# Optimization experiments

Hardware: AMD Instinct MI355X
Metric: run time of the kernel (lower is better)

## Reference

```python
import jax, jax.numpy as jnp
import numpy as np
from functools import partial

L, E, H, FF = 6, 768, 12, 3072
D = E // H
EPS = 1e-5

def _layernorm(x, g, b):
    mu = jnp.mean(x, axis=-1, keepdims=True)
    var = jnp.mean(jnp.square(x - mu), axis=-1, keepdims=True)
    return (x - mu) * jax.lax.rsqrt(var + EPS) * g + b

def setup_inputs() -> dict:
    key = jax.random.key(0)
    ks = jax.random.split(key, 16)
    s = 0.02
    return {
        "inputs_embeds": jax.random.normal(ks[0], (2, 1024, E), jnp.float32),
        "attention_mask": jnp.ones((2, 1024), jnp.float32),
        "Wqkv": jax.random.normal(ks[1], (L, E, 3 * E), jnp.float32) * s,
        "bqkv": jnp.zeros((L, 3 * E), jnp.float32),
        "Wo": jax.random.normal(ks[2], (L, E, E), jnp.float32) * s,
        "bo": jnp.zeros((L, E), jnp.float32),
        "ln1_g": jnp.ones((L, E), jnp.float32),
        "ln1_b": jnp.zeros((L, E), jnp.float32),
        "ln2_g": jnp.ones((L, E), jnp.float32),
        "ln2_b": jnp.zeros((L, E), jnp.float32),
        "Wfc": jax.random.normal(ks[3], (L, E, FF), jnp.float32) * s,
        "bfc": jnp.zeros((L, FF), jnp.float32),
        "Wmo": jax.random.normal(ks[4], (L, FF, E), jnp.float32) * s,
        "bmo": jnp.zeros((L, E), jnp.float32),
        "lnf_g": jnp.ones((E,), jnp.float32),
        "lnf_b": jnp.zeros((E,), jnp.float32),
    }

def reference(inputs_embeds, attention_mask, Wqkv, bqkv, Wo, bo,
              ln1_g, ln1_b, ln2_g, ln2_b, Wfc, bfc, Wmo, bmo, lnf_g, lnf_b):
    B, S, _ = inputs_embeds.shape
    # additive mask, broadcast over heads and query positions: [B,1,1,S]
    mask_add = (1.0 - attention_mask)[:, None, None, :] * -10000.0
    scale = 1.0 / jnp.sqrt(jnp.float32(D))

    def block(x, p):
        wqkv, bq, wo_, bo_, g1, b1, g2, b2, wfc, bf, wmo, bm = p
        h = _layernorm(x, g1, b1)
        qkv = h @ wqkv + bq                      # [B,S,3E]
        q, k, v = jnp.split(qkv, 3, axis=-1)
        q = q.reshape(B, S, H, D).transpose(0, 2, 1, 3)  # [B,H,S,D]
        k = k.reshape(B, S, H, D).transpose(0, 2, 1, 3)
        v = v.reshape(B, S, H, D).transpose(0, 2, 1, 3)
        scores = jnp.einsum('bhqd,bhkd->bhqk', q, k) * scale + mask_add
        w = jax.nn.softmax(scores, axis=-1)
        a = jnp.einsum('bhqk,bhkd->bhqd', w, v)
        a = a.transpose(0, 2, 1, 3).reshape(B, S, E)
        x = x + a @ wo_ + bo_
        m = _layernorm(x, g2, b2)
        m = jax.nn.gelu(m @ wfc + bf, approximate=False) @ wmo + bm
        x = x + m
        return x, None

    params = (Wqkv, bqkv, Wo, bo, ln1_g, ln1_b, ln2_g, ln2_b, Wfc, bfc, Wmo, bmo)
    x, _ = jax.lax.scan(block, inputs_embeds, params)
    return _layernorm(x, lnf_g, lnf_b)
```

## Files before the change

kernel.cpp:

```cpp
#include <hip/hip_runtime.h>
#include <hip/hip_bf16.h>
#include <math.h>

constexpr int LYR = 6;
constexpr int E   = 768;
constexpr int NH  = 12;
constexpr int FFD = 3072;
constexpr int HD  = 64;
constexpr int BB  = 2;
constexpr int SS  = 1024;
constexpr int T   = BB * SS;
constexpr int E3  = 3 * E;
constexpr int FH  = FFD / 2;

constexpr size_t SZ_QKV_T = (size_t)E3 * E;
constexpr size_t SZ_WO_T  = (size_t)E * E;
constexpr size_t SZ_WFC_T = (size_t)FFD * E;
constexpr size_t SZ_WMO_T = (size_t)E * FFD;
constexpr size_t LSZ      = SZ_QKV_T + SZ_WO_T + SZ_WFC_T + SZ_WMO_T;
constexpr int TQ = (E3 / 64) * (E / 64);
constexpr int TO = (E / 64) * (E / 64);
constexpr int TF = (FFD / 64) * (E / 64);
constexpr int TM = (E / 64) * (FFD / 64);
constexpr int TL = TQ + TO + TF + TM;

#define LN_EPS 1e-5f

typedef __attribute__((ext_vector_type(8))) short    short8v;
typedef __attribute__((ext_vector_type(8))) unsigned short ushort8v;
typedef __attribute__((ext_vector_type(4))) unsigned short ushort4v;
typedef __attribute__((ext_vector_type(4))) float    f32x4;

__device__ __forceinline__ float bf2f(__hip_bfloat16 x) { return __bfloat162float(x); }
__device__ __forceinline__ float bfr2f(unsigned short u) {
    union { unsigned int i; float f; } v; v.i = ((unsigned int)u) << 16; return v.f;
}
__device__ __forceinline__ __hip_bfloat16 f2bf(float f) { return __float2bfloat16(f); }
__device__ __forceinline__ unsigned short f2bfbits(float f) {
    union { float f; unsigned int i; } v; v.f = f;
    unsigned int r = (v.i + 0x7fffu + ((v.i >> 16) & 1u)) >> 16;
    return (unsigned short)r;
}

__device__ __forceinline__ float block_sum(float v, float* sm) {
    #pragma unroll
    for (int o = 32; o > 0; o >>= 1) v += __shfl_down(v, o, 64);
    int lane = threadIdx.x & 63, wid = threadIdx.x >> 6;
    if (lane == 0) sm[wid] = v;
    __syncthreads();
    float r = sm[0] + sm[1] + sm[2] + sm[3];
    __syncthreads();
    return r;
}

__device__ __forceinline__ float block_max(float v, float* sm) {
    #pragma unroll
    for (int o = 32; o > 0; o >>= 1) v = fmaxf(v, __shfl_down(v, o, 64));
    int lane = threadIdx.x & 63, wid = threadIdx.x >> 6;
    if (lane == 0) sm[wid] = v;
    __syncthreads();
    float r = fmaxf(fmaxf(sm[0], sm[1]), fmaxf(sm[2], sm[3]));
    __syncthreads();
    return r;
}

__global__ void copy4_kernel(const float4* __restrict__ in, float4* __restrict__ out, int n4) {
    int i = blockIdx.x * 256 + threadIdx.x;
    if (i < n4) out[i] = in[i];
}

__global__ void rowstat_kernel(const float* __restrict__ x, float2* __restrict__ musig) {
    __shared__ float sm[4];
    int row = blockIdx.x;
    const float* xr = x + (size_t)row * E;
    float s = 0.f;
    for (int i = threadIdx.x; i < E; i += 256) s += xr[i];
    float mu = block_sum(s, sm) * (1.0f / E);
    float v = 0.f;
    for (int i = threadIdx.x; i < E; i += 256) { float d = xr[i] - mu; v += d * d; }
    float rstd = rsqrtf(block_sum(v, sm) * (1.0f / E) + LN_EPS);
    if (threadIdx.x == 0) musig[row] = make_float2(mu, rstd);
}

template <typename OT>
__global__ void ln_kernel(const float* __restrict__ x, OT* __restrict__ out,
                          const float* __restrict__ g, const float* __restrict__ b) {
    __shared__ float sm[4];
    int row = blockIdx.x;
    const float* xr = x + (size_t)row * E;
    float s = 0.f;
    for (int i = threadIdx.x; i < E; i += 256) s += xr[i];
    float mu = block_sum(s, sm) * (1.0f / E);
    float v = 0.f;
    for (int i = threadIdx.x; i < E; i += 256) { float d = xr[i] - mu; v += d * d; }
    float rstd = rsqrtf(block_sum(v, sm) * (1.0f / E) + LN_EPS);
    for (int i = threadIdx.x; i < E; i += 256) {
        float o = (xr[i] - mu) * rstd * g[i] + b[i];
        if constexpr (sizeof(OT) == 2) out[(size_t)row * E + i] = f2bf(o);
        else                           out[(size_t)row * E + i] = o;
    }
}

__device__ __forceinline__ void transpose_tile(const float* __restrict__ W,
                                               unsigned short* __restrict__ Wt,
                                               int K, int N, int n0, int k0) {
    __shared__ float tile[32][33];
    int tx = threadIdx.x & 31, ty = threadIdx.x >> 5;
    #pragma unroll
    for (int i = 0; i < 4; i++)
        tile[ty + i * 8][tx] = W[(size_t)(k0 + ty + i * 8) * N + n0 + tx];
    __syncthreads();
    #pragma unroll
    for (int i = 0; i < 4; i++)
        Wt[(size_t)(n0 + ty + i * 8) * K + k0 + tx] = f2bfbits(tile[tx][ty + i * 8]);
}

__global__ void transpose_cvt(const float* __restrict__ W, unsigned short* __restrict__ Wt,
                              int K, int N) {
    transpose_tile(W, Wt, K, N, blockIdx.x * 32, blockIdx.y * 32);
}

__device__ __forceinline__ void transpose_tile64(const float* __restrict__ W,
                                                 unsigned short* __restrict__ Wt,
                                                 int K, int N, int n0, int k0) {
    __shared__ float tile[64][65];
    int tid = threadIdx.x;
    int rr = tid >> 4, c4 = (tid & 15) * 4;
    #pragma unroll
    for (int i = 0; i < 4; i++) {
        float4 v = *(const float4*)&W[(size_t)(k0 + rr + i * 16) * N + n0 + c4];
        tile[rr + i * 16][c4 + 0] = v.x;
        tile[rr + i * 16][c4 + 1] = v.y;
        tile[rr + i * 16][c4 + 2] = v.z;
        tile[rr + i * 16][c4 + 3] = v.w;
    }
    __syncthreads();
    int nr = tid >> 3, kc = (tid & 7) * 8;
    #pragma unroll
    for (int i = 0; i < 2; i++) {
        int n = nr + i * 32;
        ushort8v o;
        #pragma unroll
        for (int e = 0; e < 8; e++) o[e] = f2bfbits(tile[kc + e][n]);
        *(ushort8v*)&Wt[(size_t)(n0 + n) * K + k0 + kc] = o;
    }
}

__global__ void transpose_all(const float* __restrict__ Wqkv, const float* __restrict__ Wo,
                              const float* __restrict__ Wfc, const float* __restrict__ Wmo,
                              unsigned short* __restrict__ wt_all) {
    int bid = blockIdx.x;
    int layer = bid / TL, lid = bid % TL;
    unsigned short* dst = wt_all + (size_t)layer * LSZ;
    const float* W; int K, N, t;
    if (lid < TQ)                { W = Wqkv + (size_t)layer * E * E3;  K = E;   N = E3;  t = lid; }
    else if (lid < TQ + TO)      { W = Wo   + (size_t)layer * E * E;   K = E;   N = E;   t = lid - TQ;
                                   dst += SZ_QKV_T; }
    else if (lid < TQ + TO + TF) { W = Wfc  + (size_t)layer * E * FFD; K = E;   N = FFD; t = lid - TQ - TO;
                                   dst += SZ_QKV_T + SZ_WO_T; }
    else                         { W = Wmo  + (size_t)layer * FFD * E; K = FFD; N = E;   t = lid - TQ - TO - TF;
                                   dst += SZ_QKV_T + SZ_WO_T + SZ_WFC_T; }
    int nt = N / 64;
    transpose_tile64(W, dst, K, N, (t % nt) * 64, (t / nt) * 64);
}

template <int FUSE>
__global__ __launch_bounds__(512) void gemm_bt(
        const unsigned short* __restrict__ A, int lda,
        const unsigned short* __restrict__ Bt, int ldb,
        const float* __restrict__ bias,
        void* __restrict__ Cptr, int ldc, int K) {
    constexpr int BM = 64, BN = 128, PAD = 80;
    constexpr int MFR = 2, NFR = 2;
    __shared__ unsigned short As[BM * PAD];
    __shared__ unsigned short Bs[BN * PAD];

    int tid = threadIdx.x;
    int bm = blockIdx.y * BM, bn = blockIdx.x * BN;
    int kchunk = K / gridDim.z;
    int kbeg = blockIdx.z * kchunk, kend = kbeg + kchunk;
    int w = tid >> 6, lane = tid & 63, ln16 = lane & 15, q = lane >> 4;
    int wm = (w & 1) * 32, wn = (w >> 1) * 32;

    int rowA = tid >> 3, koA = (tid & 7) * 8;
    int rowB0 = tid >> 3, koB = (tid & 7) * 8;
    int rowB1 = (tid + 512) >> 3;

    f32x4 acc[MFR][NFR];
    #pragma unroll
    for (int i = 0; i < MFR; i++)
        #pragma unroll
        for (int j = 0; j < NFR; j++) acc[i][j] = (f32x4){0.f, 0.f, 0.f, 0.f};

    ushort8v aR, bR0, bR1;
    aR  = *(const ushort8v*)(A  + (size_t)(bm + rowA)  * lda + kbeg + koA);
    bR0 = *(const ushort8v*)(Bt + (size_t)(bn + rowB0) * ldb + kbeg + koB);
    bR1 = *(const ushort8v*)(Bt + (size_t)(bn + rowB1) * ldb + kbeg + koB);

    for (int k0 = kbeg; k0 < kend; k0 += 64) {
        *(ushort8v*)(&As[rowA * PAD + koA])  = aR;
        *(ushort8v*)(&Bs[rowB0 * PAD + koB]) = bR0;
        *(ushort8v*)(&Bs[rowB1 * PAD + koB]) = bR1;
        __syncthreads();

        if (k0 + 64 < kend) {
            aR  = *(const ushort8v*)(A  + (size_t)(bm + rowA)  * lda + k0 + 64 + koA);
            bR0 = *(const ushort8v*)(Bt + (size_t)(bn + rowB0) * ldb + k0 + 64 + koB);
            bR1 = *(const ushort8v*)(Bt + (size_t)(bn + rowB1) * ldb + k0 + 64 + koB);
        }

        #pragma unroll
        for (int kk = 0; kk < 64; kk += 32) {
            short8v afr[MFR], bfr[NFR];
            #pragma unroll
            for (int i = 0; i < MFR; i++)
                afr[i] = *(const short8v*)(&As[(wm + i * 16 + ln16) * PAD + kk + q * 8]);
            #pragma unroll
            for (int j = 0; j < NFR; j++)
                bfr[j] = *(const short8v*)(&Bs[(wn + j * 16 + ln16) * PAD + kk + q * 8]);
            #pragma unroll
            for (int i = 0; i < MFR; i++)
                #pragma unroll
                for (int j = 0; j < NFR; j++)
                    acc[i][j] = __builtin_amdgcn_mfma_f32_16x16x32_bf16(afr[i], bfr[j], acc[i][j], 0, 0, 0);
        }
        __syncthreads();
    }

    #pragma unroll
    for (int j = 0; j < NFR; j++) {
        int col = bn + wn + j * 16 + ln16;
        float bv = (blockIdx.z == 0) ? bias[col] : 0.f;
        #pragma unroll
        for (int i = 0; i < MFR; i++) {
            #pragma unroll
            for (int r = 0; r < 4; r++) {
                int row = bm + wm + i * 16 + q * 4 + r;
                float v = acc[i][j][r] + bv;
                if (FUSE == 1) v = 0.5f * v * (1.0f + erff(v * 0.70710678118654752f));
                if (FUSE == 0 || FUSE == 1) {
                    ((unsigned short*)Cptr)[(size_t)row * ldc + col] = f2bfbits(v);
                } else {
                    atomicAdd(&((float*)Cptr)[(size_t)row * ldc + col], v);
                }
            }
        }
    }
}

__global__ __launch_bounds__(128) void attn_mfma(unsigned short* __restrict__ qkv,
                                                 const float* __restrict__ mask) {
    constexpr int KP = 80;
    constexpr int VP = 80;
    constexpr int PP = 82;
    __shared__ unsigned short Ks[2][64 * KP];
    __shared__ unsigned short Vt[2][64 * VP];
    __shared__ unsigned short Ps[32 * PP];
    __shared__ float Ms[2][64];

    int bid = blockIdx.x;
    int qt = bid & 31;
    int h  = (bid >> 5) % NH;
    int b  = bid / (32 * NH);
    int tid = threadIdx.x;
    int w = tid >> 6, lane = tid & 63, ln16 = lane & 15, q4 = lane >> 4;

    int qrow = b * SS + qt * 32 + w * 16 + ln16;
    const unsigned short* qbase = qkv + (size_t)qrow * E3 + h * HD;
    short8v qfr0 = *(const short8v*)(qbase + q4 * 8);
    short8v qfr1 = *(const short8v*)(qbase + 32 + q4 * 8);

    ushort8v kR[4], vR[4];
    float mR = 1.0f;

    f32x4 sacc[4];
    f32x4 oacc[4];
    float m_run[4], l_run[4];
    #pragma unroll
    for (int r = 0; r < 4; r++) { m_run[r] = -1e30f; l_run[r] = 0.f; }
    #pragma unroll
    for (int i = 0; i < 4; i++) oacc[i] = (f32x4){0.f, 0.f, 0.f, 0.f};

    {
        int j0 = 0;
        #pragma unroll
        for (int i = 0; i < 4; i++) {
            int idx = tid + i * 128; int row = idx >> 3, ko = (idx & 7) * 8;
            kR[i] = *(const ushort8v*)(qkv + (size_t)(b * SS + j0 + row) * E3 + h * HD + E + ko);
        }
        #pragma unroll
        for (int i = 0; i < 4; i++) {
            int ko = (w + 2 * i) * 8;
            vR[i] = *(const ushort8v*)(qkv + (size_t)(b * SS + j0 + lane) * E3 + h * HD + 2 * E + ko);
        }
        if (tid < 64) mR = mask[b * SS + j0 + tid];
        #pragma unroll
        for (int i = 0; i < 4; i++) {
            int idx = tid + i * 128; int row = idx >> 3, ko = (idx & 7) * 8;
            *(ushort8v*)(&Ks[0][row * KP + ko]) = kR[i];
        }
        #pragma unroll
        for (int i = 0; i < 4; i++) {
            int ko = (w + 2 * i) * 8;
            #pragma unroll
            for (int e = 0; e < 8; e++)
                Vt[0][(ko + e) * VP + lane] = vR[i][e];
        }
        if (tid < 64) Ms[0][tid] = (1.0f - mR) * -10000.0f;
    }
    __syncthreads();

    for (int t = 0; t < 16; t++) {
        int cur = t & 1;
        if (t < 15) {
            int j0 = (t + 1) * 64;
            #pragma unroll
            for (int i = 0; i < 4; i++) {
                int idx = tid + i * 128; int row = idx >> 3, ko = (idx & 7) * 8;
                kR[i] = *(const ushort8v*)(qkv + (size_t)(b * SS + j0 + row) * E3 + h * HD + E + ko);
            }
            #pragma unroll
            for (int i = 0; i < 4; i++) {
                int ko = (w + 2 * i) * 8;
                vR[i] = *(const ushort8v*)(qkv + (size_t)(b * SS + j0 + lane) * E3 + h * HD + 2 * E + ko);
            }
            if (tid < 64) mR = mask[b * SS + j0 + tid];
        }

        #pragma unroll
        for (int jf = 0; jf < 4; jf++) sacc[jf] = (f32x4){0.f, 0.f, 0.f, 0.f};
        #pragma unroll
        for (int jf = 0; jf < 4; jf++) {
            short8v k0f = *(const short8v*)(&Ks[cur][(jf * 16 + ln16) * KP + q4 * 8]);
            short8v k1f = *(const short8v*)(&Ks[cur][(jf * 16 + ln16) * KP + 32 + q4 * 8]);
            sacc[jf] = __builtin_amdgcn_mfma_f32_16x16x32_bf16(qfr0, k0f, sacc[jf], 0, 0, 0);
            sacc[jf] = __builtin_amdgcn_mfma_f32_16x16x32_bf16(qfr1, k1f, sacc[jf], 0, 0, 0);
        }

        float madd[4];
        #pragma unroll
        for (int jf = 0; jf < 4; jf++) madd[jf] = Ms[cur][jf * 16 + ln16];
        #pragma unroll
        for (int jf = 0; jf < 4; jf++)
            #pragma unroll
            for (int r = 0; r < 4; r++)
                sacc[jf][r] = sacc[jf][r] * 0.125f + madd[jf];

        #pragma unroll
        for (int r = 0; r < 4; r++) {
            float mx = fmaxf(fmaxf(sacc[0][r], sacc[1][r]), fmaxf(sacc[2][r], sacc[3][r]));
            mx = fmaxf(mx, __shfl_xor(mx, 1, 64));
            mx = fmaxf(mx, __shfl_xor(mx, 2, 64));
            mx = fmaxf(mx, __shfl_xor(mx, 4, 64));
            mx = fmaxf(mx, __shfl_xor(mx, 8, 64));
            float mnew = fmaxf(m_run[r], mx);
            float alpha = __expf(m_run[r] - mnew);
            m_run[r] = mnew;
            float ps = 0.f;
            #pragma unroll
            for (int jf = 0; jf < 4; jf++) {
                float p = __expf(sacc[jf][r] - mnew);
                sacc[jf][r] = p;
                ps += p;
            }
            ps += __shfl_xor(ps, 1, 64);
            ps += __shfl_xor(ps, 2, 64);
            ps += __shfl_xor(ps, 4, 64);
            ps += __shfl_xor(ps, 8, 64);
            l_run[r] = l_run[r] * alpha + ps;
            #pragma unroll
            for (int df = 0; df < 4; df++) oacc[df][r] *= alpha;
        }

        #pragma unroll
        for (int jf = 0; jf < 4; jf++)
            #pragma unroll
            for (int r = 0; r < 4; r++)
                Ps[(w * 16 + q4 * 4 + r) * PP + jf * 16 + ln16] = f2bfbits(sacc[jf][r]);

        short8v pa0 = *(const short8v*)(&Ps[(w * 16 + ln16) * PP + q4 * 8]);
        short8v pa1 = *(const short8v*)(&Ps[(w * 16 + ln16) * PP + 32 + q4 * 8]);
        #pragma unroll
        for (int df = 0; df < 4; df++) {
            short8v v0f = *(const short8v*)(&Vt[cur][(df * 16 + ln16) * VP + q4 * 8]);
            short8v v1f = *(const short8v*)(&Vt[cur][(df * 16 + ln16) * VP + 32 + q4 * 8]);
            oacc[df] = __builtin_amdgcn_mfma_f32_16x16x32_bf16(pa0, v0f, oacc[df], 0, 0, 0);
            oacc[df] = __builtin_amdgcn_mfma_f32_16x16x32_bf16(pa1, v1f, oacc[df], 0, 0, 0);
        }

        if (t < 15) {
            int nb = cur ^ 1;
            #pragma unroll
            for (int i = 0; i < 4; i++) {
                int idx = tid + i * 128; int row = idx >> 3, ko = (idx & 7) * 8;
                *(ushort8v*)(&Ks[nb][row * KP + ko]) = kR[i];
            }
            #pragma unroll
            for (int i = 0; i < 4; i++) {
                int ko = (w + 2 * i) * 8;
                #pragma unroll
                for (int e = 0; e < 8; e++)
                    Vt[nb][(ko + e) * VP + lane] = vR[i][e];
            }
            if (tid < 64) Ms[nb][tid] = (1.0f - mR) * -10000.0f;
        }
        __syncthreads();
    }

    #pragma unroll
    for (int r = 0; r < 4; r++) {
        float inv = 1.0f / l_run[r];
        int row = b * SS + qt * 32 + w * 16 + q4 * 4 + r;
        size_t ob = (size_t)row * E3 + h * HD;
        #pragma unroll
        for (int df = 0; df < 4; df++)
            qkv[ob + df * 16 + ln16] = f2bfbits(oacc[df][r] * inv);
    }
}

template <int AMODE, int FUSE>
__global__ void gemm_mfma(const void* __restrict__ Aptr, int lda,
                          const float* __restrict__ W, int ldw,
                          const float* __restrict__ bias,
                          const float2* __restrict__ musig,
                          const float* __restrict__ lng, const float* __restrict__ lnb,
                          void* __restrict__ Cptr, int ldc, int K) {
    __shared__ unsigned short As[128 * 40];
    __shared__ unsigned short Bs[32 * 130];

    int tid = threadIdx.x;
    int bm = blockIdx.y * 128, bn = blockIdx.x * 128;
    int w = tid >> 6, lane = tid & 63, ln16 = lane & 15, q = lane >> 4;
    int wm = (w & 1) * 64, wn = (w >> 1) * 64;

    f32x4 acc[4][4];
    #pragma unroll
    for (int i = 0; i < 4; i++)
        #pragma unroll
        for (int j = 0; j < 4; j++) acc[i][j] = (f32x4){0.f, 0.f, 0.f, 0.f};

    for (int k0 = 0; k0 < K; k0 += 32) {
        if (AMODE == 0) {
            const unsigned short* A = (const unsigned short*)Aptr;
            #pragma unroll
            for (int i = 0; i < 2; i++) {
                int idx = tid + i * 256;
                int row = idx >> 2, ko = (idx & 3) * 8;
                ushort8v v = *(const ushort8v*)(A + (size_t)(bm + row) * lda + k0 + ko);
                *(ushort8v*)(&As[row * 40 + ko]) = v;
            }
        } else {
            const float* A = (const float*)Aptr;
            #pragma unroll
            for (int i = 0; i < 4; i++) {
                int idx = tid + i * 256;
                int row = idx >> 3, ko = (idx & 7) * 4;
                float4 xv = *(const float4*)(A + (size_t)(bm + row) * lda + k0 + ko);
                float2 ms = musig[bm + row];
                float4 gv = *(const float4*)(lng + k0 + ko);
                float4 bv = *(const float4*)(lnb + k0 + ko);
                ushort4v o;
                o[0] = f2bfbits((xv.x - ms.x) * ms.y * gv.x + bv.x);
                o[1] = f2bfbits((xv.y - ms.x) * ms.y * gv.y + bv.y);
                o[2] = f2bfbits((xv.z - ms.x) * ms.y * gv.z + bv.z);
                o[3] = f2bfbits((xv.w - ms.x) * ms.y * gv.w + bv.w);
                *(ushort4v*)(&As[row * 40 + ko]) = o;
            }
        }
        #pragma unroll
        for (int i = 0; i < 16; i++) {
            int idx = tid + i * 256;
            int kr = idx >> 7, n = idx & 127;
            float wv = W[(size_t)(k0 + kr) * ldw + bn + n];
            Bs[kr * 130 + n] = f2bfbits(wv);
        }
        __syncthreads();

        short8v afr[4], bfr[4];
        #pragma unroll
        for (int i = 0; i < 4; i++)
            afr[i] = *(const short8v*)(&As[(wm + i * 16 + ln16) * 40 + q * 8]);
        #pragma unroll
        for (int j = 0; j < 4; j++) {
            int n = wn + j * 16 + ln16;
            #pragma unroll
            for (int jj = 0; jj < 8; jj++)
                bfr[j][jj] = (short)Bs[(q * 8 + jj) * 130 + n];
        }
        #pragma unroll
        for (int i = 0; i < 4; i++)
            #pragma unroll
            for (int j = 0; j < 4; j++)
                acc[i][j] = __builtin_amdgcn_mfma_f32_16x16x32_bf16(afr[i], bfr[j], acc[i][j], 0, 0, 0);
        __syncthreads();
    }

    #pragma unroll
    for (int j = 0; j < 4; j++) {
        int col = bn + wn + j * 16 + ln16;
        float bv = (FUSE == 3) ? 0.f : bias[col];
        #pragma unroll
        for (int i = 0; i < 4; i++) {
            #pragma unroll
            for (int r = 0; r < 4; r++) {
                int row = bm + wm + i * 16 + q * 4 + r;
                float v = acc[i][j][r] + bv;
                if (FUSE == 1) v = 0.5f * v * (1.0f + erff(v * 0.70710678118654752f));
                if (FUSE == 0 || FUSE == 1) {
                    ((unsigned short*)Cptr)[(size_t)row * ldc + col] = f2bfbits(v);
                } else {
                    float* C = (float*)Cptr;
                    C[(size_t)row * ldc + col] += v;
                }
            }
        }
    }
}

__global__ void attn_flash(unsigned short* __restrict__ qkv,
                           const float* __restrict__ mask) {
    __shared__ float Qs[32][68];
    __shared__ float Ks[64][68];
    __shared__ float Vs[64][68];
    __shared__ float Ps[32][68];

    int bid = blockIdx.x;
    int qt = bid & 31;
    int h  = (bid >> 5) % NH;
    int b  = bid / (32 * NH);
    int tid = threadIdx.x;
    int ql = tid >> 3, grp = tid & 7;

    #pragma unroll
    for (int i = 0; i < 8; i++) {
        int idx = tid + i * 256;
        int rq = idx >> 6, d = idx & 63;
        int grow = b * SS + qt * 32 + rq;
        Qs[rq][d] = bfr2f(qkv[(size_t)grow * E3 + h * HD + d]) * 0.125f;
    }

    float m_run = -1e30f, l_run = 0.f;
    float O[8] = {0.f, 0.f, 0.f, 0.f, 0.f, 0.f, 0.f, 0.f};

    for (int c = 0; c < 16; c++) {
        int j0 = c * 64;
        #pragma unroll
        for (int i = 0; i < 4; i++) {
            int idx = tid + i * 256;
            int jj = idx >> 4, d4 = (idx & 15) * 4;
            size_t base = (size_t)(b * SS + j0 + jj) * E3 + h * HD + d4;
            ushort4v kv = *(const ushort4v*)(qkv + base + E);
            ushort4v vv = *(const ushort4v*)(qkv + base + 2 * E);
            *(float4*)&Ks[jj][d4] = make_float4(bfr2f(kv[0]), bfr2f(kv[1]), bfr2f(kv[2]), bfr2f(kv[3]));
            *(float4*)&Vs[jj][d4] = make_float4(bfr2f(vv[0]), bfr2f(vv[1]), bfr2f(vv[2]), bfr2f(vv[3]));
        }
        __syncthreads();

        float s[8] = {0.f, 0.f, 0.f, 0.f, 0.f, 0.f, 0.f, 0.f};
        #pragma unroll
        for (int d0 = 0; d0 < 64; d0 += 4) {
            float4 q4 = *(const float4*)&Qs[ql][d0];
            #pragma unroll
            for (int jl = 0; jl < 8; jl++) {
                float4 k4 = *(const float4*)&Ks[grp + jl * 8][d0];
                s[jl] += q4.x * k4.x + q4.y * k4.y + q4.z * k4.z + q4.w * k4.w;
            }
        }
        #pragma unroll
        for (int jl = 0; jl < 8; jl++)
            s[jl] += (1.0f - mask[b * SS + j0 + grp + jl * 8]) * -10000.0f;

        float cm = s[0];
        #pragma unroll
        for (int jl = 1; jl < 8; jl++) cm = fmaxf(cm, s[jl]);
        cm = fmaxf(cm, __shfl_xor(cm, 1, 64));
        cm = fmaxf(cm, __shfl_xor(cm, 2, 64));
        cm = fmaxf(cm, __shfl_xor(cm, 4, 64));

        float mnew = fmaxf(m_run, cm);
        float alpha = __expf(m_run - mnew);
        float ps = 0.f;
        #pragma unroll
        for (int jl = 0; jl < 8; jl++) {
            float p = __expf(s[jl] - mnew);
            Ps[ql][grp + jl * 8] = p;
            ps += p;
        }
        ps += __shfl_xor(ps, 1, 64);
        ps += __shfl_xor(ps, 2, 64);
        ps += __shfl_xor(ps, 4, 64);
        l_run = l_run * alpha + ps;
        m_run = mnew;
        #pragma unroll
        for (int e = 0; e < 8; e++) O[e] *= alpha;

        #pragma unroll 4
        for (int jj = 0; jj < 64; jj++) {
            float p = Ps[ql][jj];
            float4 v0 = *(const float4*)&Vs[jj][grp * 8];
            float4 v1 = *(const float4*)&Vs[jj][grp * 8 + 4];
            O[0] += p * v0.x; O[1] += p * v0.y; O[2] += p * v0.z; O[3] += p * v0.w;
            O[4] += p * v1.x; O[5] += p * v1.y; O[6] += p * v1.z; O[7] += p * v1.w;
        }
        __syncthreads();
    }

    float inv = 1.0f / l_run;
    int grow = b * SS + qt * 32 + ql;
    size_t obase = (size_t)grow * E3 + h * HD + grp * 8;
    #pragma unroll
    for (int e = 0; e < 8; e++)
        qkv[obase + e] = f2bfbits(O[e] * inv);
}

template <int FUSE, typename CT>
__global__ void gemm_legacy(const __hip_bfloat16* __restrict__ A, int lda,
                            const float* __restrict__ W, int ldw,
                            const float* __restrict__ bias,
                            CT* __restrict__ C, int ldc,
                            const float* __restrict__ resid,
                            int M, int N, int K) {
    __shared__ float As[16][65];
    __shared__ float Bs[16][65];
    int bm = blockIdx.y * 64, bn = blockIdx.x * 64;
    int tid = threadIdx.x;
    int ty = tid >> 4, tx = tid & 15;
    int ar = tid >> 2, ak = (tid & 3) << 2;
    int wk = tid >> 4, wn = (tid & 15) << 2;

    float acc[4][4] = {};
    for (int k0 = 0; k0 < K; k0 += 16) {
        ushort4 av = *(const ushort4*)(A + (size_t)(bm + ar) * lda + k0 + ak);
        As[ak + 0][ar] = bfr2f(av.x);
        As[ak + 1][ar] = bfr2f(av.y);
        As[ak + 2][ar] = bfr2f(av.z);
        As[ak + 3][ar] = bfr2f(av.w);
        float4 wv = *(const float4*)(W + (size_t)(k0 + wk) * ldw + bn + wn);
        Bs[wk][wn + 0] = wv.x;
        Bs[wk][wn + 1] = wv.y;
        Bs[wk][wn + 2] = wv.z;
        Bs[wk][wn + 3] = wv.w;
        __syncthreads();
        #pragma unroll
        for (int kk = 0; kk < 16; kk++) {
            float a[4], bv[4];
            #pragma unroll
            for (int i = 0; i < 4; i++) { a[i] = As[kk][ty * 4 + i]; bv[i] = Bs[kk][tx * 4 + i]; }
            #pragma unroll
            for (int i = 0; i < 4; i++)
                #pragma unroll
                for (int j = 0; j < 4; j++) acc[i][j] += a[i] * bv[j];
        }
        __syncthreads();
    }
    #pragma unroll
    for (int i = 0; i < 4; i++) {
        int row = bm + ty * 4 + i;
        #pragma unroll
        for (int j = 0; j < 4; j++) {
            int col = bn + tx * 4 + j;
            float v = acc[i][j];
            if (FUSE != 3) v += bias[col];
            if (FUSE == 1) v = 0.5f * v * (1.0f + erff(v * 0.70710678118654752f));
            if (FUSE == 2 || FUSE == 3) v += resid[(size_t)row * ldc + col];
            if constexpr (sizeof(CT) == 2) C[(size_t)row * ldc + col] = f2bf(v);
            else                           C[(size_t)row * ldc + col] = v;
        }
    }
}

__global__ void attn_legacy(const __hip_bfloat16* __restrict__ qkv,
                            const float* __restrict__ mask,
                            __hip_bfloat16* __restrict__ out) {
    __shared__ float sc[SS];
    __shared__ float qv[HD];
    __shared__ float oacc[4][HD];
    __shared__ float redbuf[4];

    int q = blockIdx.x & (SS - 1);
    int h = blockIdx.x >> 10;
    int tid = threadIdx.x;

    const __hip_bfloat16* qrow = qkv + (size_t)q * E3 + h * HD;
    if (tid < HD) qv[tid] = bf2f(qrow[tid]) * 0.125f;
    __syncthreads();

    for (int j = tid; j < SS; j += 256) {
        const __hip_bfloat16* krow = qkv + (size_t)j * E3 + E + h * HD;
        float d = 0.f;
        #pragma unroll
        for (int t = 0; t < HD; t += 4) {
            ushort4 kv4 = *(const ushort4*)(krow + t);
            d += qv[t] * bfr2f(kv4.x) + qv[t + 1] * bfr2f(kv4.y)
               + qv[t + 2] * bfr2f(kv4.z) + qv[t + 3] * bfr2f(kv4.w);
        }
        d += (1.0f - mask[j]) * -10000.0f;
        sc[j] = d;
    }
    __syncthreads();

    float m = -1e30f;
    for (int j = tid; j < SS; j += 256) m = fmaxf(m, sc[j]);
    m = block_max(m, redbuf);
    float s = 0.f;
    for (int j = tid; j < SS; j += 256) { float e = __expf(sc[j] - m); sc[j] = e; s += e; }
    s = block_sum(s, redbuf);
    float inv = 1.0f / s;
    __syncthreads();

    int d = tid & 63, c = tid >> 6;
    float acc = 0.f;
    int j0 = c * 256;
    for (int j = j0; j < j0 + 256; j++) {
        const __hip_bfloat16* vrow = qkv + (size_t)j * E3 + 2 * E + h * HD;
        acc += sc[j] * bf2f(vrow[d]);
    }
    oacc[c][d] = acc;
    __syncthreads();
    if (tid < HD) {
        float o = (oacc[0][tid] + oacc[1][tid] + oacc[2][tid] + oacc[3][tid]) * inv;
        out[(size_t)q * E + h * HD + tid] = f2bf(o);
    }
}

__global__ void copy_kernel(const float* __restrict__ in, float* __restrict__ out, int n) {
    int i = blockIdx.x * 256 + threadIdx.x;
    if (i < n) out[i] = in[i];
}

extern "C" void kernel_launch(void* const* d_in, const int* in_sizes, int n_in,
                              void* d_out, int out_size, void* d_ws, size_t ws_size,
                              hipStream_t stream) {
    const float* emb   = (const float*)d_in[0];
    const float* mask  = (const float*)d_in[1];
    const float* Wqkv  = (const float*)d_in[2];
    const float* bqkv  = (const float*)d_in[3];
    const float* Wo    = (const float*)d_in[4];
    const float* bo    = (const float*)d_in[5];
    const float* ln1g  = (const float*)d_in[6];
    const float* ln1b  = (const float*)d_in[7];
    const float* ln2g  = (const float*)d_in[8];
    const float* ln2b  = (const float*)d_in[9];
    const float* Wfc   = (const float*)d_in[10];
    const float* bfc   = (const float*)d_in[11];
    const float* Wmo   = (const float*)d_in[12];
    const float* bmo   = (const float*)d_in[13];
    const float* lnfg  = (const float*)d_in[14];
    const float* lnfb  = (const float*)d_in[15];

    const size_t NEED_FAST3 = sizeof(float) * (size_t)T * E
                            + 2ull * (size_t)T * E
                            + 2ull * (size_t)T * FFD
                            + 2ull * 6 * LSZ;
    const size_t NEED_FAST2 = sizeof(float) * (size_t)T * E
                            + 2ull * (size_t)T * E
                            + 2ull * (size_t)T * FFD
                            + 2ull * (size_t)E * FFD;
    const size_t NEED_FAST = sizeof(float) * (size_t)T * E
                           + 2ull * (size_t)T * E3
                           + sizeof(float2) * (size_t)T;

    if (ws_size >= NEED_FAST2) {
        const bool allw = (ws_size >= NEED_FAST3);
        float* x            = (float*)d_ws;
        unsigned short* h   = (unsigned short*)(x + (size_t)T * E);
        unsigned short* buf = h + (size_t)T * E;
        unsigned short* wt  = buf + (size_t)T * FFD;
        unsigned short* qkv = buf;
        unsigned short* ff  = buf;

        copy4_kernel<<<dim3(T * E / 4 / 256), dim3(256), 0, stream>>>(
            (const float4*)emb, (float4*)x, T * E / 4);

        if (allw) {
            transpose_all<<<dim3(6 * TL), dim3(256), 0, stream>>>(Wqkv, Wo, Wfc, Wmo, wt);
        }

        for (int l = 0; l < LYR; l++) {
            const float* wqkv_l = Wqkv + (size_t)l * E * E3;
            const float* wo_l   = Wo   + (size_t)l * E * E;
            const float* wfc_l  = Wfc  + (size_t)l * E * FFD;
            const float* wmo_l  = Wmo  + (size_t)l * FFD * E;

            const unsigned short* wq_t, *wo_t, *wfc_t, *wmo_t;
            if (allw) {
                const unsigned short* base = wt + (size_t)l * LSZ;
                wq_t  = base;
                wo_t  = base + SZ_QKV_T;
                wfc_t = base + SZ_QKV_T + SZ_WO_T;
                wmo_t = base + SZ_QKV_T + SZ_WO_T + SZ_WFC_T;
            } else {
                wq_t = wo_t = wfc_t = wmo_t = wt;
            }

            ln_kernel<__hip_bfloat16><<<dim3(T), dim3(256), 0, stream>>>(
                x, (__hip_bfloat16*)h, ln1g + l * E, ln1b + l * E);
            if (!allw)
                transpose_cvt<<<dim3(E3 / 32, E / 32), dim3(256), 0, stream>>>(wqkv_l, wt, E, E3);
            gemm_bt<0><<<dim3(E3 / 128, T / 64), dim3(512), 0, stream>>>(
                h, E, wq_t, E, bqkv + l * E3, qkv, E3, E);
            attn_mfma<<<dim3(BB * NH * 32), dim3(128), 0, stream>>>(qkv, mask);
            if (!allw)
                transpose_cvt<<<dim3(E / 32, E / 32), dim3(256), 0, stream>>>(wo_l, wt, E, E);
            gemm_bt<2><<<dim3(E / 128, T / 64, 4), dim3(512), 0, stream>>>(
                qkv, E3, wo_t, E, bo + l * E, x, E, E);

            ln_kernel<__hip_bfloat16><<<dim3(T), dim3(256), 0, stream>>>(
                x, (__hip_bfloat16*)h, ln2g + l * E, ln2b + l * E);
            if (!allw)
                transpose_cvt<<<dim3(FFD / 32, E / 32), dim3(256), 0, stream>>>(wfc_l, wt, E, FFD);
            gemm_bt<1><<<dim3(FFD / 128, T / 64), dim3(512), 0, stream>>>(
                h, E, wfc_t, E, bfc + l * FFD, ff, FFD, E);
            if (!allw)
                transpose_cvt<<<dim3(E / 32, FFD / 32), dim3(256), 0, stream>>>(wmo_l, wt, FFD, E);
            gemm_bt<2><<<dim3(E / 128, T / 64, 6), dim3(512), 0, stream>>>(
                ff, FFD, wmo_t, FFD, bmo + l * E, x, E, FFD);
        }
        ln_kernel<float><<<dim3(T), dim3(256), 0, stream>>>(x, (float*)d_out, lnfg, lnfb);
    } else if (ws_size >= NEED_FAST) {
        float* x              = (float*)d_ws;
        unsigned short* qkv   = (unsigned short*)(x + (size_t)T * E);
        float2* musig         = (float2*)(qkv + (size_t)T * E3);

        copy4_kernel<<<dim3(T * E / 4 / 256), dim3(256), 0, stream>>>(
            (const float4*)emb, (float4*)x, T * E / 4);

        for (int l = 0; l < LYR; l++) {
            const float* wqkv_l = Wqkv + (size_t)l * E * E3;
            const float* wo_l   = Wo   + (size_t)l * E * E;
            const float* wfc_l  = Wfc  + (size_t)l * E * FFD;
            const float* wmo_l  = Wmo  + (size_t)l * FFD * E;

            rowstat_kernel<<<dim3(T), dim3(256), 0, stream>>>(x, musig);
            gemm_mfma<1, 0><<<dim3(E3 / 128, T / 128), dim3(256), 0, stream>>>(
                x, E, wqkv_l, E3, bqkv + l * E3, musig, ln1g + l * E, ln1b + l * E,
                qkv, E3, E);
            attn_flash<<<dim3(BB * NH * 32), dim3(256), 0, stream>>>(qkv, mask);
            gemm_mfma<0, 2><<<dim3(E / 128, T / 128), dim3(256), 0, stream>>>(
                qkv, E3, wo_l, E, bo + l * E, nullptr, nullptr, nullptr, x, E, E);

            unsigned short* ffp = qkv;
            unsigned short* hp  = qkv + (size_t)T * FH;
            ln_kernel<__hip_bfloat16><<<dim3(T), dim3(256), 0, stream>>>(
                x, (__hip_bfloat16*)hp, ln2g + l * E, ln2b + l * E);
            for (int f = 0; f < 2; f++) {
                gemm_mfma<0, 1><<<dim3(FH / 128, T / 128), dim3(256), 0, stream>>>(
                    hp, E, wfc_l + f * FH, FFD, bfc + l * FFD + f * FH,
                    nullptr, nullptr, nullptr, ffp, FH, E);
                if (f == 0)
                    gemm_mfma<0, 3><<<dim3(E / 128, T / 128), dim3(256), 0, stream>>>(
                        ffp, FH, wmo_l + (size_t)f * FH * E, E, nullptr, nullptr, nullptr, nullptr,
                        x, E, FH);
                else
                    gemm_mfma<0, 2><<<dim3(E / 128, T / 128), dim3(256), 0, stream>>>(
                        ffp, FH, wmo_l + (size_t)f * FH * E, E, bmo + l * E, nullptr, nullptr, nullptr,
                        x, E, FH);
            }
        }
        ln_kernel<float><<<dim3(T), dim3(256), 0, stream>>>(x, (float*)d_out, lnfg, lnfb);
    } else {
        float* x           = (float*)d_ws;
        __hip_bfloat16* hb = (__hip_bfloat16*)(x + (size_t)T * E);
        __hip_bfloat16* qb = hb + (size_t)SS * E;

        int n = T * E;
        copy_kernel<<<dim3((n + 255) / 256), dim3(256), 0, stream>>>(emb, x, n);

        for (int l = 0; l < LYR; l++) {
            const float* wqkv_l = Wqkv + (size_t)l * E * E3;
            const float* wo_l   = Wo   + (size_t)l * E * E;
            const float* wfc_l  = Wfc  + (size_t)l * E * FFD;
            const float* wmo_l  = Wmo  + (size_t)l * FFD * E;

            for (int b = 0; b < BB; b++) {
                float* xb = x + (size_t)b * SS * E;
                ln_kernel<__hip_bfloat16><<<dim3(SS), dim3(256), 0, stream>>>(
                    xb, hb, ln1g + l * E, ln1b + l * E);
                gemm_legacy<0, __hip_bfloat16><<<dim3(E3 / 64, SS / 64), dim3(256), 0, stream>>>(
                    hb, E, wqkv_l, E3, bqkv + l * E3, qb, E3, nullptr, SS, E3, E);
                attn_legacy<<<dim3(NH * SS), dim3(256), 0, stream>>>(qb, mask + b * SS, hb);
                gemm_legacy<2, float><<<dim3(E / 64, SS / 64), dim3(256), 0, stream>>>(
                    hb, E, wo_l, E, bo + l * E, xb, E, xb, SS, E, E);
            }
            for (int b = 0; b < BB; b++) {
                float* xb = x + (size_t)b * SS * E;
                ln_kernel<__hip_bfloat16><<<dim3(SS), dim3(256), 0, stream>>>(
                    xb, hb, ln2g + l * E, ln2b + l * E);
                for (int f = 0; f < 2; f++) {
                    gemm_legacy<1, __hip_bfloat16><<<dim3(FH / 64, SS / 64), dim3(256), 0, stream>>>(
                        hb, E, wfc_l + f * FH, FFD, bfc + l * FFD + f * FH, qb, FH, nullptr,
                        SS, FH, E);
                    if (f == 0)
                        gemm_legacy<3, float><<<dim3(E / 64, SS / 64), dim3(256), 0, stream>>>(
                            qb, FH, wmo_l + (size_t)f * FH * E, E, nullptr, xb, E, xb, SS, E, FH);
                    else
                        gemm_legacy<2, float><<<dim3(E / 64, SS / 64), dim3(256), 0, stream>>>(
                            qb, FH, wmo_l + (size_t)f * FH * E, E, bmo + l * E, xb, E, xb, SS, E, FH);
                }
            }
        }
        ln_kernel<float><<<dim3(T), dim3(256), 0, stream>>>(x, (float*)d_out, lnfg, lnfb);
    }
}
```

Before: 1.092 ms.

## Enlarge GEMM tiles to 128x128 with 256 threads and widen weight transpose tiles

The bf16 MFMA GEMM moves from a 64x128 tile on 512 threads to a 128x128 tile on 256 threads, so each wave computes a 64x64 sub-tile with 4x4 fragments. This raises operand reuse per shared-memory load and cuts block count. Split-K factors for the output and MLP-down projections drop to match. The register prefetch of the next K slice is removed, so global loads no longer overlap with MFMA work, and the larger tiles lower occupancy. The weight transpose/convert kernel also handles 128-deep K tiles per block, halving its block count.

```diff
diff --git a/kernel.cpp b/kernel.cpp
--- a/kernel.cpp
+++ b/kernel.cpp
@@ -18,10 +18,10 @@
 constexpr size_t SZ_WFC_T = (size_t)FFD * E;
 constexpr size_t SZ_WMO_T = (size_t)E * FFD;
 constexpr size_t LSZ      = SZ_QKV_T + SZ_WO_T + SZ_WFC_T + SZ_WMO_T;
-constexpr int TQ = (E3 / 64) * (E / 64);
-constexpr int TO = (E / 64) * (E / 64);
-constexpr int TF = (FFD / 64) * (E / 64);
-constexpr int TM = (E / 64) * (FFD / 64);
+constexpr int TQ = (E3 / 64) * (E / 128);
+constexpr int TO = (E / 64) * (E / 128);
+constexpr int TF = (FFD / 64) * (E / 128);
+constexpr int TM = (E / 64) * (FFD / 128);
 constexpr int TL = TQ + TO + TF + TM;
 
 #define LN_EPS 1e-5f
@@ -120,14 +120,14 @@
     transpose_tile(W, Wt, K, N, blockIdx.x * 32, blockIdx.y * 32);
 }
 
-__device__ __forceinline__ void transpose_tile64(const float* __restrict__ W,
-                                                 unsigned short* __restrict__ Wt,
-                                                 int K, int N, int n0, int k0) {
-    __shared__ float tile[64][65];
+__device__ __forceinline__ void transpose_tile128(const float* __restrict__ W,
+                                                  unsigned short* __restrict__ Wt,
+                                                  int K, int N, int n0, int k0) {
+    __shared__ float tile[128][65];
     int tid = threadIdx.x;
     int rr = tid >> 4, c4 = (tid & 15) * 4;
     #pragma unroll
-    for (int i = 0; i < 4; i++) {
+    for (int i = 0; i < 8; i++) {
         float4 v = *(const float4*)&W[(size_t)(k0 + rr + i * 16) * N + n0 + c4];
         tile[rr + i * 16][c4 + 0] = v.x;
         tile[rr + i * 16][c4 + 1] = v.y;
@@ -135,10 +135,10 @@
         tile[rr + i * 16][c4 + 3] = v.w;
     }
     __syncthreads();
-    int nr = tid >> 3, kc = (tid & 7) * 8;
-    #pragma unroll
-    for (int i = 0; i < 2; i++) {
-        int n = nr + i * 32;
+    int nr = tid >> 4, kc = (tid & 15) * 8;
+    #pragma unroll
+    for (int i = 0; i < 4; i++) {
+        int n = nr + i * 16;
         ushort8v o;
         #pragma unroll
         for (int e = 0; e < 8; e++) o[e] = f2bfbits(tile[kc + e][n]);
@@ -161,17 +161,17 @@
     else                         { W = Wmo  + (size_t)layer * FFD * E; K = FFD; N = E;   t = lid - TQ - TO - TF;
                                    dst += SZ_QKV_T + SZ_WO_T + SZ_WFC_T; }
     int nt = N / 64;
-    transpose_tile64(W, dst, K, N, (t % nt) * 64, (t / nt) * 64);
+    transpose_tile128(W, dst, K, N, (t % nt) * 64, (t / nt) * 128);
 }
 
 template <int FUSE>
-__global__ __launch_bounds__(512) void gemm_bt(
+__global__ __launch_bounds__(256) void gemm_bt(
         const unsigned short* __restrict__ A, int lda,
         const unsigned short* __restrict__ Bt, int ldb,
         const float* __restrict__ bias,
         void* __restrict__ Cptr, int ldc, int K) {
-    constexpr int BM = 64, BN = 128, PAD = 80;
-    constexpr int MFR = 2, NFR = 2;
+    constexpr int BM = 128, BN = 128, PAD = 80;
+    constexpr int MFR = 4, NFR = 4;
     __shared__ unsigned short As[BM * PAD];
     __shared__ unsigned short Bs[BN * PAD];
 
@@ -180,11 +180,7 @@
     int kchunk = K / gridDim.z;
     int kbeg = blockIdx.z * kchunk, kend = kbeg + kchunk;
     int w = tid >> 6, lane = tid & 63, ln16 = lane & 15, q = lane >> 4;
-    int wm = (w & 1) * 32, wn = (w >> 1) * 32;
-
-    int rowA = tid >> 3, koA = (tid & 7) * 8;
-    int rowB0 = tid >> 3, koB = (tid & 7) * 8;
-    int rowB1 = (tid + 512) >> 3;
+    int wm = (w & 1) * 64, wn = (w >> 1) * 64;
 
     f32x4 acc[MFR][NFR];
     #pragma unroll
@@ -192,22 +188,22 @@
         #pragma unroll
         for (int j = 0; j < NFR; j++) acc[i][j] = (f32x4){0.f, 0.f, 0.f, 0.f};
 
-    ushort8v aR, bR0, bR1;
-    aR  = *(const ushort8v*)(A  + (size_t)(bm + rowA)  * lda + kbeg + koA);
-    bR0 = *(const ushort8v*)(Bt + (size_t)(bn + rowB0) * ldb + kbeg + koB);
-    bR1 = *(const ushort8v*)(Bt + (size_t)(bn + rowB1) * ldb + kbeg + koB);
-
     for (int k0 = kbeg; k0 < kend; k0 += 64) {
-        *(ushort8v*)(&As[rowA * PAD + koA])  = aR;
-        *(ushort8v*)(&Bs[rowB0 * PAD + koB]) = bR0;
-        *(ushort8v*)(&Bs[rowB1 * PAD + koB]) = bR1;
+        #pragma unroll
+        for (int i = 0; i < 4; i++) {
+            int idx = tid + i * 256;
+            int row = idx >> 3, ko = (idx & 7) * 8;
+            *(ushort8v*)(&As[row * PAD + ko]) =
+                *(const ushort8v*)(A + (size_t)(bm + row) * lda + k0 + ko);
+        }
+        #pragma unroll
+        for (int i = 0; i < 4; i++) {
+            int idx = tid + i * 256;
+            int row = idx >> 3, ko = (idx & 7) * 8;
+            *(ushort8v*)(&Bs[row * PAD + ko]) =
+                *(const ushort8v*)(Bt + (size_t)(bn + row) * ldb + k0 + ko);
+        }
         __syncthreads();
-
-        if (k0 + 64 < kend) {
-            aR  = *(const ushort8v*)(A  + (size_t)(bm + rowA)  * lda + k0 + 64 + koA);
-            bR0 = *(const ushort8v*)(Bt + (size_t)(bn + rowB0) * ldb + k0 + 64 + koB);
-            bR1 = *(const ushort8v*)(Bt + (size_t)(bn + rowB1) * ldb + k0 + 64 + koB);
-        }
 
         #pragma unroll
         for (int kk = 0; kk < 64; kk += 32) {
@@ -797,23 +793,23 @@
                 x, (__hip_bfloat16*)h, ln1g + l * E, ln1b + l * E);
             if (!allw)
                 transpose_cvt<<<dim3(E3 / 32, E / 32), dim3(256), 0, stream>>>(wqkv_l, wt, E, E3);
-            gemm_bt<0><<<dim3(E3 / 128, T / 64), dim3(512), 0, stream>>>(
+            gemm_bt<0><<<dim3(E3 / 128, T / 128), dim3(256), 0, stream>>>(
                 h, E, wq_t, E, bqkv + l * E3, qkv, E3, E);
             attn_mfma<<<dim3(BB * NH * 32), dim3(128), 0, stream>>>(qkv, mask);
             if (!allw)
                 transpose_cvt<<<dim3(E / 32, E / 32), dim3(256), 0, stream>>>(wo_l, wt, E, E);
-            gemm_bt<2><<<dim3(E / 128, T / 64, 4), dim3(512), 0, stream>>>(
+            gemm_bt<2><<<dim3(E / 128, T / 128, 3), dim3(256), 0, stream>>>(
                 qkv, E3, wo_t, E, bo + l * E, x, E, E);
 
             ln_kernel<__hip_bfloat16><<<dim3(T), dim3(256), 0, stream>>>(
                 x, (__hip_bfloat16*)h, ln2g + l * E, ln2b + l * E);
             if (!allw)
                 transpose_cvt<<<dim3(FFD / 32, E / 32), dim3(256), 0, stream>>>(wfc_l, wt, E, FFD);
-            gemm_bt<1><<<dim3(FFD / 128, T / 64), dim3(512), 0, stream>>>(
+            gemm_bt<1><<<dim3(FFD / 128, T / 128), dim3(256), 0, stream>>>(
                 h, E, wfc_t, E, bfc + l * FFD, ff, FFD, E);
             if (!allw)
                 transpose_cvt<<<dim3(E / 32, FFD / 32), dim3(256), 0, stream>>>(wmo_l, wt, FFD, E);
-            gemm_bt<2><<<dim3(E / 128, T / 64, 6), dim3(512), 0, stream>>>(
+            gemm_bt<2><<<dim3(E / 128, T / 128, 4), dim3(256), 0, stream>>>(
                 ff, FFD, wmo_t, FFD, bmo + l * E, x, E, FFD);
         }
         ln_kernel<float><<<dim3(T), dim3(256), 0, stream>>>(x, (float*)d_out, lnfg, lnfb);
```

Result: no change. 1.112 ms (+1.9%).
